# Optimization experiments

Measured on AMD Instinct MI355X. Metric: run time of the kernel, lower is better.

## Reference

```python
import jax, jax.numpy as jnp
import numpy as np

DIM = 64      # channels
HEADS = 2     # num_heads -> head_dim = 32
K = 7         # neighborhood kernel_size (hardcoded in module)
B, H, W = 1, 96, 96
STAGES = 3
HEAD_DIM = DIM // HEADS


def setup_inputs() -> dict:
    key = jax.random.key(0)
    ks = jax.random.split(key, 6)
    x = jax.random.normal(ks[0], (B, DIM, H, W), jnp.float32)
    qkv_w = jax.random.normal(ks[1], (STAGES, 3 * DIM, DIM), jnp.float32) * 0.02
    qkv_b = jnp.zeros((STAGES, 3 * DIM), jnp.float32)
    proj_w = jax.random.normal(ks[2], (STAGES, DIM, DIM), jnp.float32) * 0.02
    proj_b = jnp.zeros((STAGES, DIM), jnp.float32)
    rpb = jax.random.normal(ks[3], (STAGES, HEADS, 2 * K - 1, 2 * K - 1), jnp.float32) * 0.02
    return {"x": x, "qkv_w": qkv_w, "qkv_b": qkv_b, "proj_w": proj_w,
            "proj_b": proj_b, "rpb": rpb}


def _window_idx(n):
    # NATTEN-style clamped sliding windows: each query attends to exactly K keys.
    starts = jnp.clip(jnp.arange(n) - K // 2, 0, n - K)
    idx = starts[:, None] + jnp.arange(K)          # [n, K] absolute key positions
    rel = idx - jnp.arange(n)[:, None] + (K - 1)   # [n, K] rpb index in [0, 2K-2]
    return idx, rel


def _na_stage(x, qkv_w, qkv_b, proj_w, proj_b, rpb, prev_attn):
    # x: [B, H, W, C]
    b, h_, w_, c = x.shape
    qkv = x @ qkv_w.T + qkv_b                                    # [B,H,W,3C]
    qkv = qkv.reshape(b, h_, w_, 3, HEADS, HEAD_DIM)
    qkv = jnp.transpose(qkv, (3, 0, 4, 1, 2, 5))                 # [3,B,h,H,W,d]
    q, k, v = qkv[0], qkv[1], qkv[2]
    scale = HEAD_DIM ** -0.5

    idx_h, rel_h = _window_idx(h_)
    idx_w, rel_w = _window_idx(w_)

    def gather_nb(t):  # t: [B,h,H,W,d] -> [B,h,H,W,K*K,d]
        t = t[:, :, idx_h]                       # [B,h,H,K,W,d]
        t = t[:, :, :, :, idx_w]                 # [B,h,H,K,W,K,d]
        t = jnp.transpose(t, (0, 1, 2, 4, 3, 5, 6))  # [B,h,H,W,K,K,d]
        return t.reshape(b, HEADS, h_, w_, K * K, HEAD_DIM)

    k_nb = gather_nb(k)
    v_nb = gather_nb(v)

    attn = jnp.einsum('bhijd,bhijkd->bhijk', q * scale, k_nb)   # [B,h,H,W,K*K]

    # relative positional bias: rpb[head, rel_h, rel_w]
    bias = rpb[:, rel_h[:, :, None, None], rel_w[None, None, :, :]]  # [h,H,K,W,K]
    bias = jnp.transpose(bias, (0, 1, 3, 2, 4)).reshape(HEADS, h_, w_, K * K)
    attn = attn + bias[None]

    if prev_attn is not None:  # high-order chaining: previous attention map added to logits
        attn = attn + prev_attn

    attn = jax.nn.softmax(attn, axis=-1)
    out = jnp.einsum('bhijk,bhijkd->bhijd', attn, v_nb)          # [B,h,H,W,d]
    out = jnp.transpose(out, (0, 2, 3, 1, 4)).reshape(b, h_, w_, c)
    out = out @ proj_w.T + proj_b
    return out, attn


def reference(x, qkv_w, qkv_b, proj_w, proj_b, rpb):
    xh = jnp.transpose(x, (0, 2, 3, 1))  # NCHW -> NHWC
    attn = None
    for s in range(STAGES):
        xh, attn = _na_stage(xh, qkv_w[s], qkv_b[s], proj_w[s], proj_b[s], rpb[s], attn)
    return jnp.transpose(xh, (0, 3, 1, 2))  # NHWC -> NCHW
```

## Files before the change

### kernel.cpp

```cpp
#include <hip/hip_runtime.h>

#define HW 96
#define NPIX 9216
#define QN 192
#define ASTRIDE 52
#define SCALE 0.17677669529663687f
#define NT 576
#define TP 36

__device__ __forceinline__ int xswz(int row, int col) {
    return row * 64 + (((col & 60) ^ (((row >> 2) & 7) << 2)) | (col & 3));
}
__device__ __forceinline__ int wswz(int row, int col) {
    return row * 64 + (((col & 60) ^ ((row & 7) << 2)) | (col & 3));
}

__device__ __forceinline__ void qkv_gemm(const float* __restrict__ xs,
                                         const float* __restrict__ ws,
                                         const float* __restrict__ qb,
                                         float* __restrict__ qkv,
                                         int i0, int j0c, int t)
{
    const int pxg = t % 9;
    const int jo  = t / 9;
    const int jb  = jo * 3;
    float acc[4][3];
    #pragma unroll
    for (int jj = 0; jj < 3; ++jj) {
        float bv = qb[jb + jj];
        #pragma unroll
        for (int ii = 0; ii < 4; ++ii) acc[ii][jj] = bv;
    }
    #pragma unroll
    for (int cc = 0; cc < 16; ++cc) {
        float4 xv[4], wv[3];
        #pragma unroll
        for (int ii = 0; ii < 4; ++ii)
            xv[ii] = *(const float4*)&xs[xswz(pxg * 4 + ii, cc * 4)];
        #pragma unroll
        for (int jj = 0; jj < 3; ++jj)
            wv[jj] = *(const float4*)&ws[wswz(jb + jj, cc * 4)];
        #pragma unroll
        for (int ii = 0; ii < 4; ++ii)
            #pragma unroll
            for (int jj = 0; jj < 3; ++jj) {
                acc[ii][jj] = fmaf(xv[ii].x, wv[jj].x, acc[ii][jj]);
                acc[ii][jj] = fmaf(xv[ii].y, wv[jj].y, acc[ii][jj]);
                acc[ii][jj] = fmaf(xv[ii].z, wv[jj].z, acc[ii][jj]);
                acc[ii][jj] = fmaf(xv[ii].w, wv[jj].w, acc[ii][jj]);
            }
    }
    #pragma unroll
    for (int ii = 0; ii < 4; ++ii) {
        int px = pxg * 4 + ii;
        float* o = qkv + ((i0 + px / 6) * HW + j0c + px % 6) * QN + jb;
        o[0] = acc[ii][0]; o[1] = acc[ii][1]; o[2] = acc[ii][2];
    }
}

__global__ __launch_bounds__(NT) void k_qkv0(const float* __restrict__ x,
                                             const float* __restrict__ qw,
                                             const float* __restrict__ qb,
                                             float* __restrict__ qkv)
{
    __shared__ float xs[TP * 64];
    __shared__ float ws[QN * 64];
    const int t = threadIdx.x;
    const int i0 = (blockIdx.x >> 4) * 6, j0c = (blockIdx.x & 15) * 6;
    #pragma unroll
    for (int it = 0; it < 4; ++it) {
        int l = it * NT + t;
        int px = l % 36, c = l / 36;
        xs[xswz(px, c)] = x[c * NPIX + (i0 + px / 6) * HW + j0c + px % 6];
    }
    #pragma unroll
    for (int it = 0; it < 6; ++it) {
        int l = it * NT + t;
        if (l < 3072) {
            int j = l >> 4, cs = (l & 15) << 2;
            *(float4*)&ws[wswz(j, cs)] = *(const float4*)&qw[j * 64 + cs];
        }
    }
    __syncthreads();
    qkv_gemm(xs, ws, qb, qkv, i0, j0c, t);
}

template <int HASPREV, int LAST>
__global__ __launch_bounds__(NT) void k_stage(const float* __restrict__ qkv,
                                              const float* __restrict__ rpb,
                                              const float* __restrict__ prev,
                                              float* __restrict__ cur,
                                              const float* __restrict__ pw,
                                              const float* __restrict__ pb,
                                              const float* __restrict__ qw,
                                              const float* __restrict__ qb,
                                              float* __restrict__ qkvn,
                                              float* __restrict__ outp)
{
    __shared__ float xs[TP * 64];
    __shared__ float ws[QN * 64];
    __shared__ float rpb_s[338];
    const int t = threadIdx.x;
    const int i0 = (blockIdx.x >> 4) * 6, j0c = (blockIdx.x & 15) * 6;
    #pragma unroll
    for (int it = 0; it < 2; ++it) {
        int l = it * NT + t;
        if (l < 1024) {
            int j = l >> 4, cs = (l & 15) << 2;
            *(float4*)&ws[wswz(j, cs)] = *(const float4*)&pw[j * 64 + cs];
        }
    }
    if (t < 338) rpb_s[t] = rpb[t];
    const int r = t & 7, g = t >> 3;
    const int h = g & 1, pl = g >> 1;
    const int i = i0 + pl / 6, jx = j0c + pl % 6;
    const int p = i * HW + jx;
    int si = i - 3;  si = si < 0 ? 0 : (si > 89 ? 89 : si);
    int sj = jx - 3; sj = sj < 0 ? 0 : (sj > 89 ? 89 : sj);
    float4 q0;
    {
        q0 = *(const float4*)(qkv + p * QN + h * 32 + r * 4);
        q0.x *= SCALE; q0.y *= SCALE; q0.z *= SCALE; q0.w *= SCALE;
    }
    const float* kb = qkv + (si * HW + sj) * QN + 64 + h * 32 + r * 4;
    float lg[49];
    #pragma unroll
    for (int a = 0; a < 7; ++a) {
        #pragma unroll
        for (int b = 0; b < 7; ++b) {
            float4 k0 = *(const float4*)(kb + (a * HW + b) * QN);
            float s = q0.x * k0.x;
            s = fmaf(q0.y, k0.y, s); s = fmaf(q0.z, k0.z, s); s = fmaf(q0.w, k0.w, s);
            s += __shfl_xor(s, 1);
            s += __shfl_xor(s, 2);
            s += __shfl_xor(s, 4);
            lg[a * 7 + b] = s;
        }
    }
    __syncthreads();
    {
        const float* rp = rpb_s + h * 169;
        const int rh0 = si - i + 6, rw0 = sj - jx + 6;
        #pragma unroll
        for (int a = 0; a < 7; ++a)
            #pragma unroll
            for (int b = 0; b < 7; ++b)
                lg[a * 7 + b] += rp[(rh0 + a) * 13 + rw0 + b];
    }
    if (HASPREV) {
        const float4* pp = (const float4*)(prev + (p * 2 + h) * ASTRIDE);
        #pragma unroll
        for (int k = 0; k < 12; ++k) {
            float4 z = pp[k];
            lg[k * 4]     += z.x; lg[k * 4 + 1] += z.y;
            lg[k * 4 + 2] += z.z; lg[k * 4 + 3] += z.w;
        }
        lg[48] += ((const float*)pp)[48];
    }
    float mx = lg[0];
    #pragma unroll
    for (int n = 1; n < 49; ++n) mx = fmaxf(mx, lg[n]);
    float sum = 0.f;
    #pragma unroll
    for (int n = 0; n < 49; ++n) { float e = expf(lg[n] - mx); lg[n] = e; sum += e; }
    const float inv = 1.f / sum;
    #pragma unroll
    for (int n = 0; n < 49; ++n) lg[n] *= inv;
    if (!LAST && r == 0) {
        float* cb = cur + (p * 2 + h) * ASTRIDE;
        #pragma unroll
        for (int k = 0; k < 12; ++k)
            *(float4*)&cb[k * 4] = make_float4(lg[k * 4], lg[k * 4 + 1], lg[k * 4 + 2], lg[k * 4 + 3]);
        cb[48] = lg[48];
    }
    {
        float4 a0 = make_float4(0.f, 0.f, 0.f, 0.f);
        const float* vb = kb + 64;
        #pragma unroll
        for (int a = 0; a < 7; ++a) {
            #pragma unroll
            for (int b = 0; b < 7; ++b) {
                float4 v0 = *(const float4*)(vb + (a * HW + b) * QN);
                const float w0 = lg[a * 7 + b];
                a0.x = fmaf(w0, v0.x, a0.x); a0.y = fmaf(w0, v0.y, a0.y);
                a0.z = fmaf(w0, v0.z, a0.z); a0.w = fmaf(w0, v0.w, a0.w);
            }
        }
        *(float4*)&xs[xswz(pl, h * 32 + r * 4)] = a0;
    }
    __syncthreads();
    const int pxg = t % 18, jo = t / 18;
    const int jb = jo * 2;
    float pacc[2][2];
    {
        float b0 = pb[jb], b1 = pb[jb + 1];
        pacc[0][0] = b0; pacc[1][0] = b0; pacc[0][1] = b1; pacc[1][1] = b1;
    }
    #pragma unroll
    for (int cc = 0; cc < 16; ++cc) {
        float4 xv[2], wv[2];
        #pragma unroll
        for (int ii = 0; ii < 2; ++ii)
            xv[ii] = *(const float4*)&xs[xswz(pxg * 2 + ii, cc * 4)];
        #pragma unroll
        for (int jj = 0; jj < 2; ++jj)
            wv[jj] = *(const float4*)&ws[wswz(jb + jj, cc * 4)];
        #pragma unroll
        for (int ii = 0; ii < 2; ++ii)
            #pragma unroll
            for (int jj = 0; jj < 2; ++jj) {
                pacc[ii][jj] = fmaf(xv[ii].x, wv[jj].x, pacc[ii][jj]);
                pacc[ii][jj] = fmaf(xv[ii].y, wv[jj].y, pacc[ii][jj]);
                pacc[ii][jj] = fmaf(xv[ii].z, wv[jj].z, pacc[ii][jj]);
                pacc[ii][jj] = fmaf(xv[ii].w, wv[jj].w, pacc[ii][jj]);
            }
    }
    __syncthreads();
    #pragma unroll
    for (int ii = 0; ii < 2; ++ii)
        #pragma unroll
        for (int jj = 0; jj < 2; ++jj)
            xs[xswz(pxg * 2 + ii, jb + jj)] = pacc[ii][jj];
    if (!LAST) {
        #pragma unroll
        for (int it = 0; it < 6; ++it) {
            int l = it * NT + t;
            if (l < 3072) {
                int j = l >> 4, cs = (l & 15) << 2;
                *(float4*)&ws[wswz(j, cs)] = *(const float4*)&qw[j * 64 + cs];
            }
        }
    }
    __syncthreads();
    if (LAST) {
        #pragma unroll
        for (int it = 0; it < 4; ++it) {
            int l = it * NT + t;
            int px = l % 36, c = l / 36;
            outp[c * NPIX + (i0 + px / 6) * HW + j0c + px % 6] = xs[xswz(px, c)];
        }
        return;
    }
    qkv_gemm(xs, ws, qb, qkvn, i0, j0c, t);
}

extern "C" void kernel_launch(void* const* d_in, const int* in_sizes, int n_in,
                              void* d_out, int out_size, void* d_ws, size_t ws_size,
                              hipStream_t stream)
{
    const float* x   = (const float*)d_in[0];
    const float* qw  = (const float*)d_in[1];
    const float* qb  = (const float*)d_in[2];
    const float* pw  = (const float*)d_in[3];
    const float* pb  = (const float*)d_in[4];
    const float* rpb = (const float*)d_in[5];
    float* out = (float*)d_out;
    float* ws  = (float*)d_ws;

    float* qkvA = ws;
    float* qkvB = qkvA + 1769472;
    float* attA = qkvB + 1769472;
    float* attB = attA + 958464;

    k_qkv0<<<256, NT, 0, stream>>>(x, qw, qb, qkvA);
    k_stage<0, 0><<<256, NT, 0, stream>>>(qkvA, rpb,       nullptr, attA,
                                          pw,        pb,       qw + 12288, qb + 192, qkvB, nullptr);
    k_stage<1, 0><<<256, NT, 0, stream>>>(qkvB, rpb + 338, attA,    attB,
                                          pw + 4096, pb + 64,  qw + 24576, qb + 384, qkvA, nullptr);
    k_stage<1, 1><<<256, NT, 0, stream>>>(qkvA, rpb + 676, attB,    nullptr,
                                          pw + 8192, pb + 128, nullptr,    nullptr,  nullptr, out);
}
```

Baseline: 150.8 us.

## Split neighborhood attention across 16 lanes per head with swizzle-based softmax

Tiles shrink from 6x6 to 6x3 pixels, so the grid doubles to 512 blocks. Within a block, the work mapping changes: each of 16 lanes now computes full 32-dim dot products for up to 4 of the 49 neighbors instead of splitting head_dim across 8 lanes. Softmax max and sum reductions use ds_swizzle, and the PV product broadcasts weights via swizzle while each lane accumulates 2 output dims. This removes the per-neighbor shuffle reductions and the 49-element register arrays. The attention map stride becomes 64 floats, with padding lanes masked, which increases workspace traffic, and the QKV/proj GEMMs now do less reuse per thread.

```diff
diff --git a/kernel.cpp b/kernel.cpp
--- a/kernel.cpp
+++ b/kernel.cpp
@@ -3,10 +3,8 @@
 #define HW 96
 #define NPIX 9216
 #define QN 192
-#define ASTRIDE 52
 #define SCALE 0.17677669529663687f
 #define NT 576
-#define TP 36
 
 __device__ __forceinline__ int xswz(int row, int col) {
     return row * 64 + (((col & 60) ^ (((row >> 2) & 7) << 2)) | (col & 3));
@@ -14,6 +12,32 @@
 __device__ __forceinline__ int wswz(int row, int col) {
     return row * 64 + (((col & 60) ^ ((row & 7) << 2)) | (col & 3));
 }
+
+template <int PAT>
+__device__ __forceinline__ float swzf(float v) {
+    return __int_as_float(__builtin_amdgcn_ds_swizzle(__float_as_int(v), PAT));
+}
+
+template <int N>
+struct PVChain {
+    static __device__ __forceinline__ void run(const float* __restrict__ vbase,
+                                               const float* __restrict__ wk,
+                                               float& a0, float& a1, float& c0, float& c1) {
+        PVChain<N - 1>::run(vbase, wk, a0, a1, c0, c1);
+        constexpr int kn = N >> 4, ln = N & 15;
+        constexpr int av = N / 7, bv = N % 7;
+        float w = __int_as_float(__builtin_amdgcn_ds_swizzle(
+                      __float_as_int(wk[kn]), (ln << 5) | 0x10));
+        const float2 v = *(const float2*)(vbase + (av * HW + bv) * QN);
+        if (N & 1) { c0 = fmaf(w, v.x, c0); c1 = fmaf(w, v.y, c1); }
+        else       { a0 = fmaf(w, v.x, a0); a1 = fmaf(w, v.y, a1); }
+    }
+};
+template <>
+struct PVChain<-1> {
+    static __device__ __forceinline__ void run(const float*, const float*,
+                                               float&, float&, float&, float&) {}
+};
 
 __device__ __forceinline__ void qkv_gemm(const float* __restrict__ xs,
                                          const float* __restrict__ ws,
@@ -21,27 +45,25 @@
                                          float* __restrict__ qkv,
                                          int i0, int j0c, int t)
 {
-    const int pxg = t % 9;
-    const int jo  = t / 9;
-    const int jb  = jo * 3;
-    float acc[4][3];
+    const int pxg = t % 9, jo = t / 9;
+    const int jb = jo * 3;
+    float acc[2][3];
     #pragma unroll
     for (int jj = 0; jj < 3; ++jj) {
         float bv = qb[jb + jj];
-        #pragma unroll
-        for (int ii = 0; ii < 4; ++ii) acc[ii][jj] = bv;
+        acc[0][jj] = bv; acc[1][jj] = bv;
     }
     #pragma unroll
     for (int cc = 0; cc < 16; ++cc) {
-        float4 xv[4], wv[3];
-        #pragma unroll
-        for (int ii = 0; ii < 4; ++ii)
-            xv[ii] = *(const float4*)&xs[xswz(pxg * 4 + ii, cc * 4)];
+        float4 xv[2], wv[3];
+        #pragma unroll
+        for (int ii = 0; ii < 2; ++ii)
+            xv[ii] = *(const float4*)&xs[xswz(pxg * 2 + ii, cc * 4)];
         #pragma unroll
         for (int jj = 0; jj < 3; ++jj)
             wv[jj] = *(const float4*)&ws[wswz(jb + jj, cc * 4)];
         #pragma unroll
-        for (int ii = 0; ii < 4; ++ii)
+        for (int ii = 0; ii < 2; ++ii)
             #pragma unroll
             for (int jj = 0; jj < 3; ++jj) {
                 acc[ii][jj] = fmaf(xv[ii].x, wv[jj].x, acc[ii][jj]);
@@ -51,9 +73,9 @@
             }
     }
     #pragma unroll
-    for (int ii = 0; ii < 4; ++ii) {
-        int px = pxg * 4 + ii;
-        float* o = qkv + ((i0 + px / 6) * HW + j0c + px % 6) * QN + jb;
+    for (int ii = 0; ii < 2; ++ii) {
+        int px = pxg * 2 + ii;
+        float* o = qkv + ((i0 + px / 3) * HW + j0c + px % 3) * QN + jb;
         o[0] = acc[ii][0]; o[1] = acc[ii][1]; o[2] = acc[ii][2];
     }
 }
@@ -63,15 +85,15 @@
                                              const float* __restrict__ qb,
                                              float* __restrict__ qkv)
 {
-    __shared__ float xs[TP * 64];
+    __shared__ float xs[18 * 64];
     __shared__ float ws[QN * 64];
     const int t = threadIdx.x;
-    const int i0 = (blockIdx.x >> 4) * 6, j0c = (blockIdx.x & 15) * 6;
-    #pragma unroll
-    for (int it = 0; it < 4; ++it) {
+    const int i0 = (blockIdx.x >> 5) * 6, j0c = (blockIdx.x & 31) * 3;
+    #pragma unroll
+    for (int it = 0; it < 2; ++it) {
         int l = it * NT + t;
-        int px = l % 36, c = l / 36;
-        xs[xswz(px, c)] = x[c * NPIX + (i0 + px / 6) * HW + j0c + px % 6];
+        int px = l % 18, c = l / 18;
+        xs[xswz(px, c)] = x[c * NPIX + (i0 + px / 3) * HW + j0c + px % 3];
     }
     #pragma unroll
     for (int it = 0; it < 6; ++it) {
@@ -97,11 +119,10 @@
                                               float* __restrict__ qkvn,
                                               float* __restrict__ outp)
 {
-    __shared__ float xs[TP * 64];
+    __shared__ float xs[18 * 64];
     __shared__ float ws[QN * 64];
-    __shared__ float rpb_s[338];
     const int t = threadIdx.x;
-    const int i0 = (blockIdx.x >> 4) * 6, j0c = (blockIdx.x & 15) * 6;
+    const int i0 = (blockIdx.x >> 5) * 6, j0c = (blockIdx.x & 31) * 3;
     #pragma unroll
     for (int it = 0; it < 2; ++it) {
         int l = it * NT + t;
@@ -110,117 +131,93 @@
             *(float4*)&ws[wswz(j, cs)] = *(const float4*)&pw[j * 64 + cs];
         }
     }
-    if (t < 338) rpb_s[t] = rpb[t];
-    const int r = t & 7, g = t >> 3;
+    const int r = t & 15, g = t >> 4;
     const int h = g & 1, pl = g >> 1;
-    const int i = i0 + pl / 6, jx = j0c + pl % 6;
+    const int i = i0 + pl / 3, jx = j0c + pl % 3;
     const int p = i * HW + jx;
     int si = i - 3;  si = si < 0 ? 0 : (si > 89 ? 89 : si);
     int sj = jx - 3; sj = sj < 0 ? 0 : (sj > 89 ? 89 : sj);
-    float4 q0;
+    float4 q[8];
     {
-        q0 = *(const float4*)(qkv + p * QN + h * 32 + r * 4);
-        q0.x *= SCALE; q0.y *= SCALE; q0.z *= SCALE; q0.w *= SCALE;
-    }
-    const float* kb = qkv + (si * HW + sj) * QN + 64 + h * 32 + r * 4;
-    float lg[49];
-    #pragma unroll
-    for (int a = 0; a < 7; ++a) {
-        #pragma unroll
-        for (int b = 0; b < 7; ++b) {
-            float4 k0 = *(const float4*)(kb + (a * HW + b) * QN);
-            float s = q0.x * k0.x;
-            s = fmaf(q0.y, k0.y, s); s = fmaf(q0.z, k0.z, s); s = fmaf(q0.w, k0.w, s);
-            s += __shfl_xor(s, 1);
-            s += __shfl_xor(s, 2);
-            s += __shfl_xor(s, 4);
-            lg[a * 7 + b] = s;
-        }
-    }
-    __syncthreads();
+        const float4* qp = (const float4*)(qkv + p * QN + h * 32);
+        #pragma unroll
+        for (int d = 0; d < 8; ++d) q[d] = qp[d];
+    }
+    float pr[4] = {0.f, 0.f, 0.f, 0.f};
+    if (HASPREV) {
+        float4 z = *(const float4*)(prev + (p * 2 + h) * 64 + r * 4);
+        pr[0] = z.x; pr[1] = z.y; pr[2] = z.z; pr[3] = z.w;
+    }
+    const float* kbase = qkv + (si * HW + sj) * QN + 64 + h * 32;
+    float lg[4];
+    int aa[4], bb[4];
+    #pragma unroll
+    for (int k = 0; k < 4; ++k) {
+        int n = (k << 4) | r;
+        int a = (n * 147) >> 10;
+        int b = n - a * 7;
+        aa[k] = a; bb[k] = b;
+        const float4* kp = (const float4*)(kbase + (a * HW + b) * QN);
+        float s0 = 0.f, s1 = 0.f, s2 = 0.f, s3 = 0.f;
+        #pragma unroll
+        for (int d = 0; d < 8; ++d) {
+            float4 kv = kp[d];
+            s0 = fmaf(q[d].x, kv.x, s0);
+            s1 = fmaf(q[d].y, kv.y, s1);
+            s2 = fmaf(q[d].z, kv.z, s2);
+            s3 = fmaf(q[d].w, kv.w, s3);
+        }
+        lg[k] = (s0 + s1) + (s2 + s3);
+    }
     {
-        const float* rp = rpb_s + h * 169;
+        const float* rp = rpb + h * 169;
         const int rh0 = si - i + 6, rw0 = sj - jx + 6;
         #pragma unroll
-        for (int a = 0; a < 7; ++a)
-            #pragma unroll
-            for (int b = 0; b < 7; ++b)
-                lg[a * 7 + b] += rp[(rh0 + a) * 13 + rw0 + b];
-    }
-    if (HASPREV) {
-        const float4* pp = (const float4*)(prev + (p * 2 + h) * ASTRIDE);
-        #pragma unroll
-        for (int k = 0; k < 12; ++k) {
-            float4 z = pp[k];
-            lg[k * 4]     += z.x; lg[k * 4 + 1] += z.y;
-            lg[k * 4 + 2] += z.z; lg[k * 4 + 3] += z.w;
-        }
-        lg[48] += ((const float*)pp)[48];
-    }
-    float mx = lg[0];
-    #pragma unroll
-    for (int n = 1; n < 49; ++n) mx = fmaxf(mx, lg[n]);
+        for (int k = 0; k < 4; ++k) {
+            int n = (k << 4) | r;
+            float v = fmaf(lg[k], SCALE, rp[(rh0 + aa[k]) * 13 + rw0 + bb[k]] + pr[k]);
+            lg[k] = (n <= 48) ? v : -1e30f;
+        }
+    }
+    float mx = fmaxf(fmaxf(lg[0], lg[1]), fmaxf(lg[2], lg[3]));
+    mx = fmaxf(mx, swzf<0x041F>(mx));
+    mx = fmaxf(mx, swzf<0x081F>(mx));
+    mx = fmaxf(mx, swzf<0x101F>(mx));
+    mx = fmaxf(mx, swzf<0x201F>(mx));
+    float wk[4];
     float sum = 0.f;
     #pragma unroll
-    for (int n = 0; n < 49; ++n) { float e = expf(lg[n] - mx); lg[n] = e; sum += e; }
+    for (int k = 0; k < 4; ++k) { wk[k] = expf(lg[k] - mx); sum += wk[k]; }
+    sum += swzf<0x041F>(sum);
+    sum += swzf<0x081F>(sum);
+    sum += swzf<0x101F>(sum);
+    sum += swzf<0x201F>(sum);
     const float inv = 1.f / sum;
-    #pragma unroll
-    for (int n = 0; n < 49; ++n) lg[n] *= inv;
-    if (!LAST && r == 0) {
-        float* cb = cur + (p * 2 + h) * ASTRIDE;
-        #pragma unroll
-        for (int k = 0; k < 12; ++k)
-            *(float4*)&cb[k * 4] = make_float4(lg[k * 4], lg[k * 4 + 1], lg[k * 4 + 2], lg[k * 4 + 3]);
-        cb[48] = lg[48];
-    }
+    wk[0] *= inv; wk[1] *= inv; wk[2] *= inv; wk[3] *= inv;
+    if (!LAST)
+        *(float4*)(cur + (p * 2 + h) * 64 + r * 4) = make_float4(wk[0], wk[1], wk[2], wk[3]);
     {
-        float4 a0 = make_float4(0.f, 0.f, 0.f, 0.f);
-        const float* vb = kb + 64;
-        #pragma unroll
-        for (int a = 0; a < 7; ++a) {
-            #pragma unroll
-            for (int b = 0; b < 7; ++b) {
-                float4 v0 = *(const float4*)(vb + (a * HW + b) * QN);
-                const float w0 = lg[a * 7 + b];
-                a0.x = fmaf(w0, v0.x, a0.x); a0.y = fmaf(w0, v0.y, a0.y);
-                a0.z = fmaf(w0, v0.z, a0.z); a0.w = fmaf(w0, v0.w, a0.w);
-            }
-        }
-        *(float4*)&xs[xswz(pl, h * 32 + r * 4)] = a0;
-    }
-    __syncthreads();
-    const int pxg = t % 18, jo = t / 18;
-    const int jb = jo * 2;
-    float pacc[2][2];
-    {
-        float b0 = pb[jb], b1 = pb[jb + 1];
-        pacc[0][0] = b0; pacc[1][0] = b0; pacc[0][1] = b1; pacc[1][1] = b1;
-    }
+        const float* vbase = qkv + (si * HW + sj) * QN + 128 + h * 32 + r * 2;
+        float a0 = 0.f, a1 = 0.f, c0 = 0.f, c1 = 0.f;
+        PVChain<48>::run(vbase, wk, a0, a1, c0, c1);
+        *(float2*)&xs[xswz(pl, h * 32 + r * 2)] = make_float2(a0 + c0, a1 + c1);
+    }
+    __syncthreads();
+    const int pxg = t % 9, jo = t / 9;
+    float pa0 = pb[jo], pa1 = pa0;
     #pragma unroll
     for (int cc = 0; cc < 16; ++cc) {
-        float4 xv[2], wv[2];
-        #pragma unroll
-        for (int ii = 0; ii < 2; ++ii)
-            xv[ii] = *(const float4*)&xs[xswz(pxg * 2 + ii, cc * 4)];
-        #pragma unroll
-        for (int jj = 0; jj < 2; ++jj)
-            wv[jj] = *(const float4*)&ws[wswz(jb + jj, cc * 4)];
-        #pragma unroll
-        for (int ii = 0; ii < 2; ++ii)
-            #pragma unroll
-            for (int jj = 0; jj < 2; ++jj) {
-                pacc[ii][jj] = fmaf(xv[ii].x, wv[jj].x, pacc[ii][jj]);
-                pacc[ii][jj] = fmaf(xv[ii].y, wv[jj].y, pacc[ii][jj]);
-                pacc[ii][jj] = fmaf(xv[ii].z, wv[jj].z, pacc[ii][jj]);
-                pacc[ii][jj] = fmaf(xv[ii].w, wv[jj].w, pacc[ii][jj]);
-            }
-    }
-    __syncthreads();
-    #pragma unroll
-    for (int ii = 0; ii < 2; ++ii)
-        #pragma unroll
-        for (int jj = 0; jj < 2; ++jj)
-            xs[xswz(pxg * 2 + ii, jb + jj)] = pacc[ii][jj];
+        float4 xv0 = *(const float4*)&xs[xswz(pxg * 2, cc * 4)];
+        float4 xv1 = *(const float4*)&xs[xswz(pxg * 2 + 1, cc * 4)];
+        float4 wv  = *(const float4*)&ws[wswz(jo, cc * 4)];
+        pa0 = fmaf(xv0.x, wv.x, pa0); pa0 = fmaf(xv0.y, wv.y, pa0);
+        pa0 = fmaf(xv0.z, wv.z, pa0); pa0 = fmaf(xv0.w, wv.w, pa0);
+        pa1 = fmaf(xv1.x, wv.x, pa1); pa1 = fmaf(xv1.y, wv.y, pa1);
+        pa1 = fmaf(xv1.z, wv.z, pa1); pa1 = fmaf(xv1.w, wv.w, pa1);
+    }
+    __syncthreads();
+    xs[xswz(pxg * 2, jo)]     = pa0;
+    xs[xswz(pxg * 2 + 1, jo)] = pa1;
     if (!LAST) {
         #pragma unroll
         for (int it = 0; it < 6; ++it) {
@@ -234,10 +231,10 @@
     __syncthreads();
     if (LAST) {
         #pragma unroll
-        for (int it = 0; it < 4; ++it) {
+        for (int it = 0; it < 2; ++it) {
             int l = it * NT + t;
-            int px = l % 36, c = l / 36;
-            outp[c * NPIX + (i0 + px / 6) * HW + j0c + px % 6] = xs[xswz(px, c)];
+            int px = l % 18, c = l / 18;
+            outp[c * NPIX + (i0 + px / 3) * HW + j0c + px % 3] = xs[xswz(px, c)];
         }
         return;
     }
@@ -260,13 +257,13 @@
     float* qkvA = ws;
     float* qkvB = qkvA + 1769472;
     float* attA = qkvB + 1769472;
-    float* attB = attA + 958464;
-
-    k_qkv0<<<256, NT, 0, stream>>>(x, qw, qb, qkvA);
-    k_stage<0, 0><<<256, NT, 0, stream>>>(qkvA, rpb,       nullptr, attA,
+    float* attB = attA + 1179648;
+
+    k_qkv0<<<512, NT, 0, stream>>>(x, qw, qb, qkvA);
+    k_stage<0, 0><<<512, NT, 0, stream>>>(qkvA, rpb,       nullptr, attA,
                                           pw,        pb,       qw + 12288, qb + 192, qkvB, nullptr);
-    k_stage<1, 0><<<256, NT, 0, stream>>>(qkvB, rpb + 338, attA,    attB,
+    k_stage<1, 0><<<512, NT, 0, stream>>>(qkvB, rpb + 338, attA,    attB,
                                           pw + 4096, pb + 64,  qw + 24576, qb + 384, qkvA, nullptr);
-    k_stage<1, 1><<<256, NT, 0, stream>>>(qkvA, rpb + 676, attB,    nullptr,
+    k_stage<1, 1><<<512, NT, 0, stream>>>(qkvA, rpb + 676, attB,    nullptr,
                                           pw + 8192, pb + 128, nullptr,    nullptr,  nullptr, out);
 }
```

After: 185.7 us. 23.2% more time.
